# Optimization experiments

Hardware: AMD Instinct MI355X
Metric: run time of the kernel (lower is better)

Reference implementation:

```python
import jax, jax.numpy as jnp
import numpy as np

TEMPERATURE = 0.05
EPS = 1e-8  # torch CosineSimilarity eps


def setup_inputs() -> dict:
    key = jax.random.key(0)
    k1, k2, k3 = jax.random.split(key, 3)
    B2, S, D, P = 2048, 64, 512, 256
    representations = jax.random.normal(k1, (B2, S, D), dtype=jnp.float32)
    input_lengths = jax.random.randint(k2, (B2,), 1, S + 1)  # valid lengths in [1, S]
    proj_w = jax.random.normal(k3, (P, D), dtype=jnp.float32) / np.sqrt(D).astype(np.float32)
    proj_b = jnp.zeros((P,), dtype=jnp.float32)
    return {"representations": representations, "input_lengths": input_lengths,
            "proj_w": proj_w, "proj_b": proj_b}


def reference(representations, proj_w, proj_b, input_lengths):
    # Gather the representation at the last valid timestep of each sequence.
    N, S, D = representations.shape
    idx = jnp.clip(input_lengths - 1, 0, S - 1)
    traj_reps = representations[jnp.arange(N), idx]            # [2B, D]
    # model.projection (Linear D -> P)
    proj = traj_reps @ proj_w.T + proj_b                       # [2B, P]
    B = N // 2
    # Cosine similarity == row-normalize then GEMM (fused form of the
    # original broadcasted unsqueeze version).
    norm = jnp.maximum(jnp.linalg.norm(proj, axis=-1, keepdims=True), EPS)
    z = proj / norm
    z1, z2 = z[:B], z[B:]
    inv_t = 1.0 / TEMPERATURE
    sim11 = (z1 @ z1.T) * inv_t                                # [B, B]
    sim22 = (z2 @ z2.T) * inv_t
    sim12 = (z1 @ z2.T) * inv_t
    eye = jnp.eye(B, dtype=bool)
    neg_inf = jnp.float32(-jnp.inf)
    sim11 = jnp.where(eye, neg_inf, sim11)
    sim22 = jnp.where(eye, neg_inf, sim22)
    logits = jnp.concatenate(
        [jnp.concatenate([sim12, sim11], axis=-1),
         jnp.concatenate([sim22, sim12.T], axis=-1)], axis=0)  # [2B, 2B]
    labels = jnp.arange(2 * B)
    # CrossEntropyLoss with labels == diagonal indices
    lse = jax.nn.logsumexp(logits, axis=-1)
    ce_loss = jnp.mean(lse - logits[labels, labels])
    return ce_loss
```

## Files before the change

kernel.cpp:

```cpp
#include <hip/hip_runtime.h>
#include <math.h>


#define NROWS 2048
#define DDIM  512
#define PDIM  256
static constexpr float INV_T = 20.0f;
static constexpr float EPSN  = 1e-8f;

__global__ __launch_bounds__(256) void k_proj(const float* __restrict__ rep,
                                              const int*   __restrict__ lens,
                                              const float* __restrict__ W,
                                              const float* __restrict__ bias,
                                              float* __restrict__ z) {
  __shared__ float A[4][512];
  __shared__ float Wl[32][257];
  __shared__ float red[4][4];

  const int t   = threadIdx.x;
  const int blk = blockIdx.x;

  for (int i = 0; i < 2; ++i) {
    int e = i * 256 + t;
    int r = e >> 7;
    int q = e & 127;
    int n = blk * 4 + r;
    int idx = lens[n] - 1;
    idx = idx < 0 ? 0 : (idx > 63 ? 63 : idx);
    const float4* src = (const float4*)(rep + ((size_t)(n * 64 + idx)) * 512);
    ((float4*)&A[r][0])[q] = src[q];
  }

  const int p = t;
  float acc[4];
  {
    float bv = bias[p];
    for (int r = 0; r < 4; ++r) acc[r] = bv;
  }

  const float4* W4 = (const float4*)W;
  for (int kc = 0; kc < DDIM; kc += 32) {
    __syncthreads();
    for (int i = 0; i < 8; ++i) {
      int idx = i * 256 + t;
      int pp = idx >> 3;
      int dq = idx & 7;
      float4 w = W4[(size_t)pp * 128 + (kc >> 2) + dq];
      Wl[dq * 4 + 0][pp] = w.x;
      Wl[dq * 4 + 1][pp] = w.y;
      Wl[dq * 4 + 2][pp] = w.z;
      Wl[dq * 4 + 3][pp] = w.w;
    }
    __syncthreads();
    for (int d4 = 0; d4 < 8; ++d4) {
      float w0 = Wl[d4 * 4 + 0][p];
      float w1 = Wl[d4 * 4 + 1][p];
      float w2 = Wl[d4 * 4 + 2][p];
      float w3 = Wl[d4 * 4 + 3][p];
      for (int r = 0; r < 4; ++r) {
        float4 av = *(const float4*)&A[r][kc + d4 * 4];
        acc[r] += av.x * w0 + av.y * w1 + av.z * w2 + av.w * w3;
      }
    }
  }

  const int wid = t >> 6, lane = t & 63;
  for (int r = 0; r < 4; ++r) {
    float v = acc[r] * acc[r];
    for (int off = 32; off >= 1; off >>= 1) v += __shfl_xor(v, off, 64);
    if (lane == 0) red[r][wid] = v;
  }
  __syncthreads();
  for (int r = 0; r < 4; ++r) {
    float ss = red[r][0] + red[r][1] + red[r][2] + red[r][3];
    float nrm = sqrtf(ss);
    nrm = nrm < EPSN ? EPSN : nrm;
    z[(size_t)(blk * 4 + r) * 256 + p] = acc[r] / nrm;
  }
}

__global__ __launch_bounds__(256) void k_gram(const float* __restrict__ z,
                                              float* __restrict__ mPart,
                                              float* __restrict__ sPart) {
  __shared__ float Zr[64][36];
  __shared__ float Zc[64][36];
  __shared__ float cred[2][4][16][4];

  const int t = threadIdx.x;
  int b = blockIdx.x;
  int I = 0;
  while (b >= 32 - I) { b -= 32 - I; ++I; }
  const int J = I + b;
  const int rb = I * 64;
  const int cb = J * 64;
  const int tx = t & 15, ty = t >> 4;
  const int wv = t >> 6;

  float acc[4][4];
  for (int i = 0; i < 4; ++i)
    for (int j = 0; j < 4; ++j) acc[i][j] = 0.0f;

  const float4* z4 = (const float4*)z;
  for (int kc = 0; kc < PDIM; kc += 32) {
    __syncthreads();
    for (int i = 0; i < 2; ++i) {
      int idx = i * 256 + t;
      int row = idx >> 3;
      int dq  = idx & 7;
      *(float4*)&Zr[row][dq * 4] = z4[(size_t)(rb + row) * 64 + (kc >> 2) + dq];
      *(float4*)&Zc[row][dq * 4] = z4[(size_t)(cb + row) * 64 + (kc >> 2) + dq];
    }
    __syncthreads();
    for (int d4 = 0; d4 < 32; d4 += 4) {
      float4 a0 = *(const float4*)&Zr[ty +  0][d4];
      float4 a1 = *(const float4*)&Zr[ty + 16][d4];
      float4 a2 = *(const float4*)&Zr[ty + 32][d4];
      float4 a3 = *(const float4*)&Zr[ty + 48][d4];
      float4 b0 = *(const float4*)&Zc[tx +  0][d4];
      float4 b1 = *(const float4*)&Zc[tx + 16][d4];
      float4 b2 = *(const float4*)&Zc[tx + 32][d4];
      float4 b3 = *(const float4*)&Zc[tx + 48][d4];
#define DOT4(u, v) (u.x * v.x + u.y * v.y + u.z * v.z + u.w * v.w)
      acc[0][0] += DOT4(a0, b0); acc[0][1] += DOT4(a0, b1);
      acc[0][2] += DOT4(a0, b2); acc[0][3] += DOT4(a0, b3);
      acc[1][0] += DOT4(a1, b0); acc[1][1] += DOT4(a1, b1);
      acc[1][2] += DOT4(a1, b2); acc[1][3] += DOT4(a1, b3);
      acc[2][0] += DOT4(a2, b0); acc[2][1] += DOT4(a2, b1);
      acc[2][2] += DOT4(a2, b2); acc[2][3] += DOT4(a2, b3);
      acc[3][0] += DOT4(a3, b0); acc[3][1] += DOT4(a3, b1);
      acc[3][2] += DOT4(a3, b2); acc[3][3] += DOT4(a3, b3);
#undef DOT4
    }
  }

  float v[4][4];
  for (int ri = 0; ri < 4; ++ri) {
    const int grow = rb + ty + 16 * ri;
    for (int ci = 0; ci < 4; ++ci) {
      const int gcol = cb + tx + 16 * ci;
      v[ri][ci] = (grow == gcol) ? -INFINITY : acc[ri][ci] * INV_T;
    }
  }

  for (int ri = 0; ri < 4; ++ri) {
    const int grow = rb + ty + 16 * ri;
    float m = -INFINITY;
    for (int ci = 0; ci < 4; ++ci) m = fmaxf(m, v[ri][ci]);
    for (int off = 1; off < 16; off <<= 1) m = fmaxf(m, __shfl_xor(m, off, 64));
    float s = 0.0f;
    for (int ci = 0; ci < 4; ++ci)
      s += (v[ri][ci] == -INFINITY) ? 0.0f : __expf(v[ri][ci] - m);
    for (int off = 1; off < 16; off <<= 1) s += __shfl_xor(s, off, 64);
    if (tx == 0) {
      mPart[(size_t)grow * 32 + J] = m;
      sPart[(size_t)grow * 32 + J] = s;
    }
  }

  if (I != J) {
    float cm[4];
    for (int ci = 0; ci < 4; ++ci) {
      float m = v[0][ci];
      for (int ri = 1; ri < 4; ++ri) m = fmaxf(m, v[ri][ci]);
      m = fmaxf(m, __shfl_xor(m, 16, 64));
      m = fmaxf(m, __shfl_xor(m, 32, 64));
      cm[ci] = m;
    }
    if ((t & 48) == 0)
      for (int ci = 0; ci < 4; ++ci) cred[0][wv][tx][ci] = cm[ci];
    __syncthreads();
    float M[4];
    for (int ci = 0; ci < 4; ++ci) {
      float m = cred[0][0][tx][ci];
      for (int w = 1; w < 4; ++w) m = fmaxf(m, cred[0][w][tx][ci]);
      M[ci] = m;
    }
    float cs[4];
    for (int ci = 0; ci < 4; ++ci) {
      float s = 0.0f;
      for (int ri = 0; ri < 4; ++ri) s += __expf(v[ri][ci] - M[ci]);
      s += __shfl_xor(s, 16, 64);
      s += __shfl_xor(s, 32, 64);
      cs[ci] = s;
    }
    if ((t & 48) == 0)
      for (int ci = 0; ci < 4; ++ci) cred[1][wv][tx][ci] = cs[ci];
    __syncthreads();
    if (t < 16) {
      for (int ci = 0; ci < 4; ++ci) {
        float s = cred[1][0][tx][ci] + cred[1][1][tx][ci] +
                  cred[1][2][tx][ci] + cred[1][3][tx][ci];
        const int gcol = cb + tx + 16 * ci;
        mPart[(size_t)gcol * 32 + I] = M[ci];
        sPart[(size_t)gcol * 32 + I] = s;
      }
    }
  }
}

__global__ __launch_bounds__(256) void k_finish(const float* __restrict__ z,
                                                const float* __restrict__ mPart,
                                                const float* __restrict__ sPart,
                                                float* __restrict__ out) {
  __shared__ float red[4];
  const int t = threadIdx.x;
  const int wid = t >> 6, lane = t & 63;
  const int row = blockIdx.x * 4 + wid;

  float m = (lane < 32) ? mPart[(size_t)row * 32 + lane] : -INFINITY;
  float s = (lane < 32) ? sPart[(size_t)row * 32 + lane] : 0.0f;
  float M = m;
  for (int off = 1; off < 64; off <<= 1) M = fmaxf(M, __shfl_xor(M, off, 64));
  float se = (lane < 32) ? s * __expf(m - M) : 0.0f;
  for (int off = 1; off < 64; off <<= 1) se += __shfl_xor(se, off, 64);
  float lse = M + logf(se);

  const int partner = row < 1024 ? row + 1024 : row - 1024;
  float4 a = ((const float4*)(z + (size_t)row * 256))[lane];
  float4 b = ((const float4*)(z + (size_t)partner * 256))[lane];
  float d = a.x * b.x + a.y * b.y + a.z * b.z + a.w * b.w;
  for (int off = 1; off < 64; off <<= 1) d += __shfl_xor(d, off, 64);

  if (lane == 0) red[wid] = lse - d * INV_T;
  __syncthreads();
  if (t == 0)
    atomicAdd(out, (red[0] + red[1] + red[2] + red[3]) * (1.0f / 2048.0f));
}

extern "C" void kernel_launch(void* const* d_in, const int* in_sizes, int n_in,
                              void* d_out, int out_size, void* d_ws, size_t ws_size,
                              hipStream_t stream) {
  const float* rep  = (const float*)d_in[0];
  const int*   lens = (const int*)  d_in[1];
  const float* W    = (const float*)d_in[2];
  const float* bias = (const float*)d_in[3];
  float* out = (float*)d_out;

  float* z     = (float*)d_ws;
  float* mPart = z + NROWS * PDIM;
  float* sPart = mPart + NROWS * 32;

  hipMemsetAsync(d_out, 0, sizeof(float), stream);
  k_proj  <<<512, 256, 0, stream>>>(rep, lens, W, bias, z);
  k_gram  <<<528, 256, 0, stream>>>(z, mPart, sPart);
  k_finish<<<512, 256, 0, stream>>>(z, mPart, sPart, out);
}
```

Before: 425.3 us.

## Prefetch next K-tile into registers and widen projection blocks to 512 threads

Both the projection and Gram kernels now load the next K-chunk from global memory into registers while computing on the current shared-memory tile, which overlaps global load latency with FMA work. The projection kernel processes 8 rows per 512-thread block, so each W tile staged in shared memory is reused across twice as many rows. The output zeroing moves into k_proj, replacing the separate hipMemsetAsync launch. This costs more registers and halves the projection grid to 256 blocks, which may lower occupancy and load balance across CUs.

```diff
diff --git a/kernel.cpp b/kernel.cpp
--- a/kernel.cpp
+++ b/kernel.cpp
@@ -8,30 +8,35 @@
 static constexpr float INV_T = 20.0f;
 static constexpr float EPSN  = 1e-8f;
 
-__global__ __launch_bounds__(256) void k_proj(const float* __restrict__ rep,
+__global__ __launch_bounds__(512) void k_proj(const float* __restrict__ rep,
                                               const int*   __restrict__ lens,
                                               const float* __restrict__ W,
                                               const float* __restrict__ bias,
-                                              float* __restrict__ z) {
-  __shared__ float A[4][512];
+                                              float* __restrict__ z,
+                                              float* __restrict__ out) {
+  __shared__ float A[8][512];
   __shared__ float Wl[32][257];
-  __shared__ float red[4][4];
+  __shared__ float red[8][4];
 
   const int t   = threadIdx.x;
   const int blk = blockIdx.x;
 
+  if (blk == 0 && t == 0) out[0] = 0.0f;
+
   for (int i = 0; i < 2; ++i) {
-    int e = i * 256 + t;
+    int e = i * 512 + t;
     int r = e >> 7;
     int q = e & 127;
-    int n = blk * 4 + r;
+    int n = blk * 8 + r;
     int idx = lens[n] - 1;
     idx = idx < 0 ? 0 : (idx > 63 ? 63 : idx);
     const float4* src = (const float4*)(rep + ((size_t)(n * 64 + idx)) * 512);
     ((float4*)&A[r][0])[q] = src[q];
   }
 
-  const int p = t;
+  const int p    = t & 255;
+  const int half = t >> 8;
+
   float acc[4];
   {
     float bv = bias[p];
@@ -39,28 +44,51 @@
   }
 
   const float4* W4 = (const float4*)W;
+  int pp[4], dq[4];
+  for (int i = 0; i < 4; ++i) {
+    int idx = i * 512 + t;
+    pp[i] = idx >> 3;
+    dq[i] = idx & 7;
+  }
+
+  float4 wreg[4];
+  for (int i = 0; i < 4; ++i)
+    wreg[i] = W4[(size_t)pp[i] * 128 + dq[i]];
+  __syncthreads();
+  for (int i = 0; i < 4; ++i) {
+    Wl[dq[i] * 4 + 0][pp[i]] = wreg[i].x;
+    Wl[dq[i] * 4 + 1][pp[i]] = wreg[i].y;
+    Wl[dq[i] * 4 + 2][pp[i]] = wreg[i].z;
+    Wl[dq[i] * 4 + 3][pp[i]] = wreg[i].w;
+  }
+  __syncthreads();
+
   for (int kc = 0; kc < DDIM; kc += 32) {
-    __syncthreads();
-    for (int i = 0; i < 8; ++i) {
-      int idx = i * 256 + t;
-      int pp = idx >> 3;
-      int dq = idx & 7;
-      float4 w = W4[(size_t)pp * 128 + (kc >> 2) + dq];
-      Wl[dq * 4 + 0][pp] = w.x;
-      Wl[dq * 4 + 1][pp] = w.y;
-      Wl[dq * 4 + 2][pp] = w.z;
-      Wl[dq * 4 + 3][pp] = w.w;
-    }
-    __syncthreads();
+    const bool more = (kc + 32) < DDIM;
+    if (more) {
+      int kq = (kc + 32) >> 2;
+      for (int i = 0; i < 4; ++i)
+        wreg[i] = W4[(size_t)pp[i] * 128 + kq + dq[i]];
+    }
     for (int d4 = 0; d4 < 8; ++d4) {
       float w0 = Wl[d4 * 4 + 0][p];
       float w1 = Wl[d4 * 4 + 1][p];
       float w2 = Wl[d4 * 4 + 2][p];
       float w3 = Wl[d4 * 4 + 3][p];
       for (int r = 0; r < 4; ++r) {
-        float4 av = *(const float4*)&A[r][kc + d4 * 4];
+        float4 av = *(const float4*)&A[half * 4 + r][kc + d4 * 4];
         acc[r] += av.x * w0 + av.y * w1 + av.z * w2 + av.w * w3;
       }
+    }
+    if (more) {
+      __syncthreads();
+      for (int i = 0; i < 4; ++i) {
+        Wl[dq[i] * 4 + 0][pp[i]] = wreg[i].x;
+        Wl[dq[i] * 4 + 1][pp[i]] = wreg[i].y;
+        Wl[dq[i] * 4 + 2][pp[i]] = wreg[i].z;
+        Wl[dq[i] * 4 + 3][pp[i]] = wreg[i].w;
+      }
+      __syncthreads();
     }
   }
 
@@ -68,14 +96,15 @@
   for (int r = 0; r < 4; ++r) {
     float v = acc[r] * acc[r];
     for (int off = 32; off >= 1; off >>= 1) v += __shfl_xor(v, off, 64);
-    if (lane == 0) red[r][wid] = v;
+    if (lane == 0) red[half * 4 + r][wid & 3] = v;
   }
   __syncthreads();
   for (int r = 0; r < 4; ++r) {
-    float ss = red[r][0] + red[r][1] + red[r][2] + red[r][3];
+    const int grow = half * 4 + r;
+    float ss = red[grow][0] + red[grow][1] + red[grow][2] + red[grow][3];
     float nrm = sqrtf(ss);
     nrm = nrm < EPSN ? EPSN : nrm;
-    z[(size_t)(blk * 4 + r) * 256 + p] = acc[r] / nrm;
+    z[(size_t)(blk * 8 + grow) * 256 + p] = acc[r] / nrm;
   }
 }
 
@@ -101,16 +130,33 @@
     for (int j = 0; j < 4; ++j) acc[i][j] = 0.0f;
 
   const float4* z4 = (const float4*)z;
+  int srow[2], sdq[2];
+  for (int i = 0; i < 2; ++i) {
+    int idx = i * 256 + t;
+    srow[i] = idx >> 3;
+    sdq[i]  = idx & 7;
+  }
+
+  float4 rreg[2], creg[2];
+  for (int i = 0; i < 2; ++i) {
+    rreg[i] = z4[(size_t)(rb + srow[i]) * 64 + sdq[i]];
+    creg[i] = z4[(size_t)(cb + srow[i]) * 64 + sdq[i]];
+  }
+  for (int i = 0; i < 2; ++i) {
+    *(float4*)&Zr[srow[i]][sdq[i] * 4] = rreg[i];
+    *(float4*)&Zc[srow[i]][sdq[i] * 4] = creg[i];
+  }
+  __syncthreads();
+
   for (int kc = 0; kc < PDIM; kc += 32) {
-    __syncthreads();
-    for (int i = 0; i < 2; ++i) {
-      int idx = i * 256 + t;
-      int row = idx >> 3;
-      int dq  = idx & 7;
-      *(float4*)&Zr[row][dq * 4] = z4[(size_t)(rb + row) * 64 + (kc >> 2) + dq];
-      *(float4*)&Zc[row][dq * 4] = z4[(size_t)(cb + row) * 64 + (kc >> 2) + dq];
-    }
-    __syncthreads();
+    const bool more = (kc + 32) < PDIM;
+    if (more) {
+      int kq = (kc + 32) >> 2;
+      for (int i = 0; i < 2; ++i) {
+        rreg[i] = z4[(size_t)(rb + srow[i]) * 64 + kq + sdq[i]];
+        creg[i] = z4[(size_t)(cb + srow[i]) * 64 + kq + sdq[i]];
+      }
+    }
     for (int d4 = 0; d4 < 32; d4 += 4) {
       float4 a0 = *(const float4*)&Zr[ty +  0][d4];
       float4 a1 = *(const float4*)&Zr[ty + 16][d4];
@@ -131,6 +177,14 @@
       acc[3][2] += DOT4(a3, b2); acc[3][3] += DOT4(a3, b3);
 #undef DOT4
     }
+    if (more) {
+      __syncthreads();
+      for (int i = 0; i < 2; ++i) {
+        *(float4*)&Zr[srow[i]][sdq[i] * 4] = rreg[i];
+        *(float4*)&Zc[srow[i]][sdq[i] * 4] = creg[i];
+      }
+      __syncthreads();
+    }
   }
 
   float v[4][4];
@@ -240,8 +294,7 @@
   float* mPart = z + NROWS * PDIM;
   float* sPart = mPart + NROWS * 32;
 
-  hipMemsetAsync(d_out, 0, sizeof(float), stream);
-  k_proj  <<<512, 256, 0, stream>>>(rep, lens, W, bias, z);
+  k_proj  <<<256, 512, 0, stream>>>(rep, lens, W, bias, z, out);
   k_gram  <<<528, 256, 0, stream>>>(z, mPart, sPart);
   k_finish<<<512, 256, 0, stream>>>(z, mPart, sPart, out);
 }
```

Result: faster. 380.1 us (-10.6%).

## Double-buffer projection and gram tiles, widen k_proj blocks, drop memset

Applied to the files above, without the earlier changes.

k_proj now uses 512-thread blocks that each handle 8 rows. Each wave stages its own 32 output columns of W in a private double-buffered LDS slice, so the main loop needs no block-wide barriers and every block re-reads W half as often. k_gram prefetches the next K chunk into registers while computing on the current LDS buffer, cutting one barrier per chunk. The output zeroing moves into k_proj, replacing the separate memset call. The cost is more LDS per block and fewer blocks, which may lower occupancy.

```diff
diff --git a/kernel.cpp b/kernel.cpp
--- a/kernel.cpp
+++ b/kernel.cpp
@@ -8,82 +8,116 @@
 static constexpr float INV_T = 20.0f;
 static constexpr float EPSN  = 1e-8f;
 
-__global__ __launch_bounds__(256) void k_proj(const float* __restrict__ rep,
+__global__ __launch_bounds__(512) void k_proj(const float* __restrict__ rep,
                                               const int*   __restrict__ lens,
                                               const float* __restrict__ W,
                                               const float* __restrict__ bias,
-                                              float* __restrict__ z) {
-  __shared__ float A[4][512];
-  __shared__ float Wl[32][257];
-  __shared__ float red[4][4];
+                                              float* __restrict__ z,
+                                              float* __restrict__ out) {
+  __shared__ float A[8][512];
+  __shared__ float Wl[2][16][257];
+  __shared__ float red[8][8];
 
   const int t   = threadIdx.x;
   const int blk = blockIdx.x;
 
+  if (blk == 0 && t == 0) out[0] = 0.0f;
+
   for (int i = 0; i < 2; ++i) {
-    int e = i * 256 + t;
+    int e = i * 512 + t;
     int r = e >> 7;
     int q = e & 127;
-    int n = blk * 4 + r;
+    int n = blk * 8 + r;
     int idx = lens[n] - 1;
     idx = idx < 0 ? 0 : (idx > 63 ? 63 : idx);
     const float4* src = (const float4*)(rep + ((size_t)(n * 64 + idx)) * 512);
     ((float4*)&A[r][0])[q] = src[q];
   }
 
-  const int p = t;
+  const int w    = t >> 6;
+  const int lane = t & 63;
+  const int l31  = lane & 31;
+  const int half = lane >> 5;
+  const int p    = w * 32 + l31;
+
   float acc[4];
   {
     float bv = bias[p];
     for (int r = 0; r < 4; ++r) acc[r] = bv;
   }
 
+  const int sc0 = lane >> 2,        sq0 = lane & 3;
+  const int sc1 = 16 + (lane >> 2), sq1 = lane & 3;
   const float4* W4 = (const float4*)W;
-  for (int kc = 0; kc < DDIM; kc += 32) {
-    __syncthreads();
-    for (int i = 0; i < 8; ++i) {
-      int idx = i * 256 + t;
-      int pp = idx >> 3;
-      int dq = idx & 7;
-      float4 w = W4[(size_t)pp * 128 + (kc >> 2) + dq];
-      Wl[dq * 4 + 0][pp] = w.x;
-      Wl[dq * 4 + 1][pp] = w.y;
-      Wl[dq * 4 + 2][pp] = w.z;
-      Wl[dq * 4 + 3][pp] = w.w;
-    }
-    __syncthreads();
-    for (int d4 = 0; d4 < 8; ++d4) {
-      float w0 = Wl[d4 * 4 + 0][p];
-      float w1 = Wl[d4 * 4 + 1][p];
-      float w2 = Wl[d4 * 4 + 2][p];
-      float w3 = Wl[d4 * 4 + 3][p];
+  const size_t wbase0 = (size_t)(w * 32 + sc0) * 128 + sq0;
+  const size_t wbase1 = (size_t)(w * 32 + sc1) * 128 + sq1;
+  const int col0 = w * 32 + sc0, col1 = w * 32 + sc1;
+
+  float4 wr0 = W4[wbase0];
+  float4 wr1 = W4[wbase1];
+  __syncthreads();
+
+  Wl[0][sq0 * 4 + 0][col0] = wr0.x;
+  Wl[0][sq0 * 4 + 1][col0] = wr0.y;
+  Wl[0][sq0 * 4 + 2][col0] = wr0.z;
+  Wl[0][sq0 * 4 + 3][col0] = wr0.w;
+  Wl[0][sq1 * 4 + 0][col1] = wr1.x;
+  Wl[0][sq1 * 4 + 1][col1] = wr1.y;
+  Wl[0][sq1 * 4 + 2][col1] = wr1.z;
+  Wl[0][sq1 * 4 + 3][col1] = wr1.w;
+
+  for (int ci = 0; ci < 32; ++ci) {
+    const int kc = ci << 4;
+    if (ci < 31) {
+      const size_t kq = (size_t)(ci + 1) << 2;
+      wr0 = W4[wbase0 + kq];
+      wr1 = W4[wbase1 + kq];
+    }
+    const float (*Wb)[257] = Wl[ci & 1];
+    for (int d4 = 0; d4 < 4; ++d4) {
+      float w0 = Wb[d4 * 4 + 0][p];
+      float w1 = Wb[d4 * 4 + 1][p];
+      float w2 = Wb[d4 * 4 + 2][p];
+      float w3 = Wb[d4 * 4 + 3][p];
       for (int r = 0; r < 4; ++r) {
-        float4 av = *(const float4*)&A[r][kc + d4 * 4];
+        float4 av = *(const float4*)&A[half * 4 + r][kc + d4 * 4];
         acc[r] += av.x * w0 + av.y * w1 + av.z * w2 + av.w * w3;
       }
     }
-  }
-
-  const int wid = t >> 6, lane = t & 63;
+    if (ci < 31) {
+      float (*Wn)[257] = Wl[(ci + 1) & 1];
+      Wn[sq0 * 4 + 0][col0] = wr0.x;
+      Wn[sq0 * 4 + 1][col0] = wr0.y;
+      Wn[sq0 * 4 + 2][col0] = wr0.z;
+      Wn[sq0 * 4 + 3][col0] = wr0.w;
+      Wn[sq1 * 4 + 0][col1] = wr1.x;
+      Wn[sq1 * 4 + 1][col1] = wr1.y;
+      Wn[sq1 * 4 + 2][col1] = wr1.z;
+      Wn[sq1 * 4 + 3][col1] = wr1.w;
+    }
+  }
+
   for (int r = 0; r < 4; ++r) {
     float v = acc[r] * acc[r];
-    for (int off = 32; off >= 1; off >>= 1) v += __shfl_xor(v, off, 64);
-    if (lane == 0) red[r][wid] = v;
+    for (int off = 1; off < 32; off <<= 1) v += __shfl_xor(v, off, 64);
+    if (l31 == 0) red[half * 4 + r][w] = v;
   }
   __syncthreads();
   for (int r = 0; r < 4; ++r) {
-    float ss = red[r][0] + red[r][1] + red[r][2] + red[r][3];
+    const int g = half * 4 + r;
+    float ss = red[g][0] + red[g][1] + red[g][2] + red[g][3] +
+               red[g][4] + red[g][5] + red[g][6] + red[g][7];
     float nrm = sqrtf(ss);
     nrm = nrm < EPSN ? EPSN : nrm;
-    z[(size_t)(blk * 4 + r) * 256 + p] = acc[r] / nrm;
+    z[(size_t)(blk * 8 + g) * 256 + p] = acc[r] / nrm;
   }
 }
 
 __global__ __launch_bounds__(256) void k_gram(const float* __restrict__ z,
                                               float* __restrict__ mPart,
                                               float* __restrict__ sPart) {
-  __shared__ float Zr[64][36];
-  __shared__ float Zc[64][36];
+  __shared__ float Zr[2][64][36];
+  __shared__ float Zc[2][64][36];
   __shared__ float cred[2][4][16][4];
 
   const int t = threadIdx.x;
@@ -101,25 +135,39 @@
     for (int j = 0; j < 4; ++j) acc[i][j] = 0.0f;
 
   const float4* z4 = (const float4*)z;
-  for (int kc = 0; kc < PDIM; kc += 32) {
-    __syncthreads();
-    for (int i = 0; i < 2; ++i) {
-      int idx = i * 256 + t;
-      int row = idx >> 3;
-      int dq  = idx & 7;
-      *(float4*)&Zr[row][dq * 4] = z4[(size_t)(rb + row) * 64 + (kc >> 2) + dq];
-      *(float4*)&Zc[row][dq * 4] = z4[(size_t)(cb + row) * 64 + (kc >> 2) + dq];
-    }
-    __syncthreads();
+  const int srow0 = t >> 3,        sdq0 = t & 7;
+  const int srow1 = 32 + (t >> 3), sdq1 = t & 7;
+
+  float4 rr0, rr1, cr0, cr1;
+  rr0 = z4[(size_t)(rb + srow0) * 64 + sdq0];
+  rr1 = z4[(size_t)(rb + srow1) * 64 + sdq1];
+  cr0 = z4[(size_t)(cb + srow0) * 64 + sdq0];
+  cr1 = z4[(size_t)(cb + srow1) * 64 + sdq1];
+  *(float4*)&Zr[0][srow0][sdq0 * 4] = rr0;
+  *(float4*)&Zr[0][srow1][sdq1 * 4] = rr1;
+  *(float4*)&Zc[0][srow0][sdq0 * 4] = cr0;
+  *(float4*)&Zc[0][srow1][sdq1 * 4] = cr1;
+  __syncthreads();
+
+  for (int c = 0; c < 8; ++c) {
+    if (c < 7) {
+      const size_t kq = (size_t)(c + 1) * 8;
+      rr0 = z4[(size_t)(rb + srow0) * 64 + kq + sdq0];
+      rr1 = z4[(size_t)(rb + srow1) * 64 + kq + sdq1];
+      cr0 = z4[(size_t)(cb + srow0) * 64 + kq + sdq0];
+      cr1 = z4[(size_t)(cb + srow1) * 64 + kq + sdq1];
+    }
+    const float (*ZrC)[36] = Zr[c & 1];
+    const float (*ZcC)[36] = Zc[c & 1];
     for (int d4 = 0; d4 < 32; d4 += 4) {
-      float4 a0 = *(const float4*)&Zr[ty +  0][d4];
-      float4 a1 = *(const float4*)&Zr[ty + 16][d4];
-      float4 a2 = *(const float4*)&Zr[ty + 32][d4];
-      float4 a3 = *(const float4*)&Zr[ty + 48][d4];
-      float4 b0 = *(const float4*)&Zc[tx +  0][d4];
-      float4 b1 = *(const float4*)&Zc[tx + 16][d4];
-      float4 b2 = *(const float4*)&Zc[tx + 32][d4];
-      float4 b3 = *(const float4*)&Zc[tx + 48][d4];
+      float4 a0 = *(const float4*)&ZrC[ty +  0][d4];
+      float4 a1 = *(const float4*)&ZrC[ty + 16][d4];
+      float4 a2 = *(const float4*)&ZrC[ty + 32][d4];
+      float4 a3 = *(const float4*)&ZrC[ty + 48][d4];
+      float4 b0 = *(const float4*)&ZcC[tx +  0][d4];
+      float4 b1 = *(const float4*)&ZcC[tx + 16][d4];
+      float4 b2 = *(const float4*)&ZcC[tx + 32][d4];
+      float4 b3 = *(const float4*)&ZcC[tx + 48][d4];
 #define DOT4(u, v) (u.x * v.x + u.y * v.y + u.z * v.z + u.w * v.w)
       acc[0][0] += DOT4(a0, b0); acc[0][1] += DOT4(a0, b1);
       acc[0][2] += DOT4(a0, b2); acc[0][3] += DOT4(a0, b3);
@@ -130,6 +178,15 @@
       acc[3][0] += DOT4(a3, b0); acc[3][1] += DOT4(a3, b1);
       acc[3][2] += DOT4(a3, b2); acc[3][3] += DOT4(a3, b3);
 #undef DOT4
+    }
+    if (c < 7) {
+      float (*ZrN)[36] = Zr[(c + 1) & 1];
+      float (*ZcN)[36] = Zc[(c + 1) & 1];
+      *(float4*)&ZrN[srow0][sdq0 * 4] = rr0;
+      *(float4*)&ZrN[srow1][sdq1 * 4] = rr1;
+      *(float4*)&ZcN[srow0][sdq0 * 4] = cr0;
+      *(float4*)&ZcN[srow1][sdq1 * 4] = cr1;
+      __syncthreads();
     }
   }
 
@@ -240,8 +297,7 @@
   float* mPart = z + NROWS * PDIM;
   float* sPart = mPart + NROWS * 32;
 
-  hipMemsetAsync(d_out, 0, sizeof(float), stream);
-  k_proj  <<<512, 256, 0, stream>>>(rep, lens, W, bias, z);
+  k_proj  <<<256, 512, 0, stream>>>(rep, lens, W, bias, z, out);
   k_gram  <<<528, 256, 0, stream>>>(z, mPart, sPart);
   k_finish<<<512, 256, 0, stream>>>(z, mPart, sPart, out);
 }
```

Measured after the change: 380.1 us. 1.12x faster.
